# Kernel tuning notes

Measured on AMD Instinct MI355X. Metric: run time of the kernel, lower is better.

Reference implementation:

```python
import jax, jax.numpy as jnp
import numpy as np

B, T, C = 4, 2048, 1024
N_HEAD = 16
HS = C // N_HEAD  # head_size = 64


def setup_inputs() -> dict:
    key = jax.random.key(0)
    k1, k2, k3 = jax.random.split(key, 3)
    x = jax.random.normal(k1, (B, T, C), dtype=jnp.float32)
    # torch Linear(in, out, bias=False); stored here as (in, out) so y = x @ W
    W_attn = jax.random.normal(k2, (C, 3 * C), dtype=jnp.float32) * (C ** -0.5)
    W_proj = jax.random.normal(k3, (C, C), dtype=jnp.float32) * (C ** -0.5)
    return {"x": x, "W_attn": W_attn, "W_proj": W_proj}


def reference(x, W_attn, W_proj):
    Bq, Tq, Cq = x.shape
    qkv = x @ W_attn                              # (B, T, 3C)
    q, k, v = jnp.split(qkv, 3, axis=-1)          # each (B, T, C)
    # (B, T, C) -> (B, H, T, hs)
    q = q.reshape(Bq, Tq, N_HEAD, HS).transpose(0, 2, 1, 3)
    k = k.reshape(Bq, Tq, N_HEAD, HS).transpose(0, 2, 1, 3)
    v = v.reshape(Bq, Tq, N_HEAD, HS).transpose(0, 2, 1, 3)
    scale = HS ** -0.5
    att = jnp.einsum("bhqd,bhkd->bhqk", q, k) * scale  # (B, H, T, T)
    causal = jnp.tril(jnp.ones((Tq, Tq), dtype=bool))
    att = jnp.where(causal[None, None], att, jnp.finfo(att.dtype).min)
    att = jax.nn.softmax(att, axis=-1)
    y = jnp.einsum("bhqk,bhkd->bhqd", att, v)     # (B, H, T, hs)
    y = y.transpose(0, 2, 1, 3).reshape(Bq, Tq, Cq)
    return y @ W_proj                             # (B, T, C)
```

## Files before the change

kernel.cpp:

```cpp
#include <hip/hip_runtime.h>
#include <stdint.h>

typedef __bf16 bf16x8 __attribute__((ext_vector_type(8)));
typedef float f32x4 __attribute__((ext_vector_type(4)));

__device__ __forceinline__ unsigned short f2bf(float f) {
  unsigned u = __builtin_bit_cast(unsigned, f);
  u = (u + 0x7fffu + ((u >> 16) & 1u)) >> 16;
  return (unsigned short)u;
}

__device__ __forceinline__ unsigned cvt_pk_bf16(float a, float b) {
  unsigned r;
  asm("v_cvt_pk_bf16_f32 %0, %1, %2" : "=v"(r) : "v"(a), "v"(b));
  return r;
}

__device__ __forceinline__ void gload_lds16(const unsigned short* g, unsigned short* l) {
  __builtin_amdgcn_global_load_lds(
      (__attribute__((address_space(1))) unsigned int*)g,
      (__attribute__((address_space(3))) unsigned int*)l, 16, 0, 0);
}

__device__ __forceinline__ void store_val(float* p, float v) { *p = v; }
__device__ __forceinline__ void store_val(unsigned short* p, float v) { *p = f2bf(v); }

__device__ __forceinline__ void transpose_tile(const float* __restrict__ in,
                                               unsigned short* __restrict__ out,
                                               int R, int Ccols, float qscale, int qcols,
                                               int bxx, int byy,
                                               unsigned short (*t)[65]) {
  int r0 = byy * 64, c0 = bxx * 64;
  int tid = threadIdx.x;
#pragma unroll
  for (int rep = 0; rep < 16; rep++) {
    int idx = rep * 256 + tid;
    int rr = idx >> 6, cc = idx & 63;
    float v = in[(size_t)(r0 + rr) * Ccols + c0 + cc];
    if (c0 + cc < qcols) v *= qscale;
    t[rr][cc] = f2bf(v);
  }
  __syncthreads();
#pragma unroll
  for (int rep = 0; rep < 16; rep++) {
    int idx = rep * 256 + tid;
    int cc = idx >> 6, rr = idx & 63;
    out[(size_t)(c0 + cc) * R + r0 + rr] = t[rr][cc];
  }
}

__global__ __launch_bounds__(256) void prep_kernel(const float* __restrict__ x,
                                                   unsigned short* __restrict__ xb,
                                                   const float* __restrict__ Wa,
                                                   unsigned short* __restrict__ Wta,
                                                   const float* __restrict__ Wp,
                                                   unsigned short* __restrict__ Wtp,
                                                   float SC) {
  __shared__ unsigned short t[64][65];
  int bx = blockIdx.x;
  if (bx < 2048) {
    const int n = 8192 * 1024;
    const int stride = 2048 * 256 * 4;
    for (int i = (bx * 256 + threadIdx.x) * 4; i < n; i += stride) {
      float4 v = *(const float4*)(x + i);
      ushort4 o;
      o.x = f2bf(v.x); o.y = f2bf(v.y); o.z = f2bf(v.z); o.w = f2bf(v.w);
      *(ushort4*)(xb + i) = o;
    }
  } else if (bx < 2816) {
    int idx = bx - 2048;
    transpose_tile(Wa, Wta, 1024, 3072, SC, 1024, idx % 48, idx / 48, t);
  } else {
    int idx = bx - 2816;
    transpose_tile(Wp, Wtp, 1024, 1024, 1.0f, 0, idx % 16, idx / 16, t);
  }
}

template <typename OutT, bool WRITEV>
__global__ __launch_bounds__(512, 2) void gemm_bt(const unsigned short* __restrict__ A,
                                                  const unsigned short* __restrict__ Bt,
                                                  OutT* __restrict__ C, int M, int N, int K,
                                                  int mtiles, unsigned short* __restrict__ vt) {
  __shared__ unsigned short lds3[3][24576];
  const int tid = threadIdx.x;
  const int wid = tid >> 6, l = tid & 63;
  const int wm = wid >> 2, wn = wid & 3;
  const int lr = l & 15, lg = l >> 4;

  int nwg = gridDim.x;
  int q8 = nwg >> 3;
  int bid = blockIdx.x;
  int bs = (bid & 7) * q8 + (bid >> 3);
  int mt = bs % mtiles, nt = bs / mtiles;
  const int m0 = mt * 128, n0 = nt * 256;

  const int srow = tid >> 3;
  const int schunk = ((tid & 7) ^ (srow & 7)) * 8;
  const unsigned short* gA0 = A + (size_t)(m0 + srow) * K + schunk;
  const unsigned short* gB0 = Bt + (size_t)(n0 + srow) * K + schunk;
  const int wslice = wid * 512;

  int arow[4], brow[2][2], xoff[2];
#pragma unroll
  for (int m = 0; m < 4; m++) arow[m] = (wm * 64 + m * 16 + lr) * 64;
#pragma unroll
  for (int qq = 0; qq < 2; qq++)
#pragma unroll
    for (int j = 0; j < 2; j++) brow[qq][j] = 8192 + (wn * 64 + qq * 32 + j * 16 + lr) * 64;
#pragma unroll
  for (int ks = 0; ks < 2; ks++) xoff[ks] = ((ks * 4 + lg) ^ (lr & 7)) * 8;

  f32x4 acc[4][4] = {};
  const int NT = K >> 6;

  gload_lds16(gA0, &lds3[0][wslice]);
  gload_lds16(gA0 + (size_t)64 * K, &lds3[0][4096 + wslice]);
#pragma unroll
  for (int u = 0; u < 4; u++)
    gload_lds16(gB0 + (size_t)(u * 64) * K, &lds3[0][8192 + u * 4096 + wslice]);
  gload_lds16(gA0 + 64, &lds3[1][wslice]);
  gload_lds16(gA0 + (size_t)64 * K + 64, &lds3[1][4096 + wslice]);
#pragma unroll
  for (int u = 0; u < 4; u++)
    gload_lds16(gB0 + (size_t)(u * 64) * K + 64, &lds3[1][8192 + u * 4096 + wslice]);

  int cb = 0;
  for (int t = 0; t < NT; t++) {
    if (t == NT - 1) {
      asm volatile("s_waitcnt vmcnt(0)" ::: "memory");
    } else {
      asm volatile("s_waitcnt vmcnt(6)" ::: "memory");
    }
    __builtin_amdgcn_s_barrier();
    const unsigned short* bufc = lds3[cb];
    int pb = cb + 2; if (pb >= 3) pb -= 3;
    unsigned short* bufp = lds3[pb];
    const int k2 = (t + 2) * 64;
    const bool pre = (t + 2) < NT;

    if (pre) {
      gload_lds16(gA0 + k2, bufp + wslice);
      gload_lds16(gA0 + (size_t)64 * K + k2, bufp + 4096 + wslice);
      gload_lds16(gB0 + k2, bufp + 8192 + wslice);
    }
    bf16x8 af[4][2];
#pragma unroll
    for (int m = 0; m < 4; m++)
#pragma unroll
      for (int ks = 0; ks < 2; ks++)
        af[m][ks] = *(const bf16x8*)&bufc[arow[m] + xoff[ks]];
    {
      bf16x8 bq[2][2];
#pragma unroll
      for (int j = 0; j < 2; j++)
#pragma unroll
        for (int ks = 0; ks < 2; ks++)
          bq[j][ks] = *(const bf16x8*)&bufc[brow[0][j] + xoff[ks]];
      __builtin_amdgcn_s_setprio(1);
#pragma unroll
      for (int m = 0; m < 4; m++)
#pragma unroll
        for (int j = 0; j < 2; j++)
#pragma unroll
          for (int ks = 0; ks < 2; ks++)
            acc[m][j] = __builtin_amdgcn_mfma_f32_16x16x32_bf16(af[m][ks], bq[j][ks], acc[m][j], 0, 0, 0);
      __builtin_amdgcn_s_setprio(0);
    }
    if (pre) {
      gload_lds16(gB0 + (size_t)64 * K + k2, bufp + 12288 + wslice);
      gload_lds16(gB0 + (size_t)128 * K + k2, bufp + 16384 + wslice);
      gload_lds16(gB0 + (size_t)192 * K + k2, bufp + 20480 + wslice);
    }
    {
      bf16x8 bq[2][2];
#pragma unroll
      for (int j = 0; j < 2; j++)
#pragma unroll
        for (int ks = 0; ks < 2; ks++)
          bq[j][ks] = *(const bf16x8*)&bufc[brow[1][j] + xoff[ks]];
      __builtin_amdgcn_s_setprio(1);
#pragma unroll
      for (int m = 0; m < 4; m++)
#pragma unroll
        for (int j = 0; j < 2; j++)
#pragma unroll
          for (int ks = 0; ks < 2; ks++)
            acc[m][2 + j] = __builtin_amdgcn_mfma_f32_16x16x32_bf16(af[m][ks], bq[j][ks], acc[m][2 + j], 0, 0, 0);
      __builtin_amdgcn_s_setprio(0);
    }
    cb = (cb == 2) ? 0 : cb + 1;
  }

  if (WRITEV && n0 >= 2048) {
    int hh = ((n0 - 2048) >> 6) + wn;
#pragma unroll
    for (int m = 0; m < 4; m++) {
      int row = m0 + wm * 64 + m * 16 + lg * 4;
      int bb = row >> 11, tt = row & 2047;
      size_t base = (size_t)(bb * 16 + hh) * 131072 + tt;
#pragma unroll
      for (int n = 0; n < 4; n++) {
        int d = n * 16 + lr;
        ushort4 v;
        v.x = f2bf(acc[m][n][0]); v.y = f2bf(acc[m][n][1]);
        v.z = f2bf(acc[m][n][2]); v.w = f2bf(acc[m][n][3]);
        *(ushort4*)&vt[base + (size_t)d * 2048] = v;
      }
    }
  } else {
#pragma unroll
    for (int m = 0; m < 4; m++)
#pragma unroll
      for (int n = 0; n < 4; n++)
#pragma unroll
        for (int i = 0; i < 4; i++) {
          size_t row = (size_t)(m0 + wm * 64 + m * 16 + lg * 4 + i);
          size_t col = (size_t)(n0 + wn * 64 + n * 16 + lr);
          store_val(&C[row * N + col], acc[m][n][i]);
        }
  }
}

__global__ __launch_bounds__(256, 3) void attn_kernel(const unsigned short* __restrict__ qkv,
                                                      const unsigned short* __restrict__ vt,
                                                      unsigned short* __restrict__ y) {
  __shared__ unsigned short k_lds[2][64 * 64];
  __shared__ unsigned short v_lds[2][64 * 64];
  __shared__ unsigned short p_lds[8][16 * 64];
  int tid = threadIdx.x;
  int w = tid >> 6, l = tid & 63;
  int lr = l & 15, lg = l >> 4;
  int g4 = lg * 4;
  int lband = l & 48;
  int bh = blockIdx.x;
  int b = bh >> 4, h = bh & 15;
  int qgrp = 15 - blockIdx.y;
  int q0 = qgrp * 128 + w * 32;

  char* plo = (char*)p_lds[w * 2];
  char* phi = (char*)p_lds[w * 2 + 1];

  int srow = tid >> 3;
  int schunk = (tid & 7) ^ (srow & 7);
  const unsigned short* gK0 = qkv + (size_t)(b * 2048 + srow) * 3072 + 1024 + h * 64 + schunk * 8;
  const unsigned short* gK1 = gK0 + (size_t)32 * 3072;
  const unsigned short* gV0 = vt + (size_t)bh * 131072 + (size_t)srow * 2048 + schunk * 8;
  const unsigned short* gV1 = gV0 + (size_t)32 * 2048;
  int ldsbase0 = w * 512;
  int ldsbase1 = 2048 + w * 512;

  const unsigned short* qp = qkv + (size_t)(b * 2048 + q0 + lr) * 3072 + h * 64 + lg * 8;
  bf16x8 aQ0lo = *(const bf16x8*)qp;
  bf16x8 aQ1lo = *(const bf16x8*)(qp + 32);
  bf16x8 aQ0hi = *(const bf16x8*)(qp + 16 * 3072);
  bf16x8 aQ1hi = *(const bf16x8*)(qp + 16 * 3072 + 32);

  f32x4 Olo[4] = {}, Ohi[4] = {};
  float sumlo = 0.f, sumhi = 0.f;

  int rx = lr & 7;
  int kc0 = (lg ^ rx) * 8;
  int kc1 = ((4 + lg) ^ rx) * 8;

  int nbmax = ((qgrp * 128 + 96) >> 6) + 1;
  int kend = q0 + 31;
  int kdiag = q0 >> 6;

  gload_lds16(gK0, &k_lds[0][ldsbase0]);
  gload_lds16(gK1, &k_lds[0][ldsbase1]);
  gload_lds16(gV0, &v_lds[0][ldsbase0]);
  gload_lds16(gV1, &v_lds[0][ldsbase1]);
  __syncthreads();

  int cur = 0;
  for (int kb = 0; kb < nbmax; kb++) {
    int kbase = kb * 64;
    if (kb + 1 < nbmax) {
      size_t koff = (size_t)(kbase + 64) * 3072;
      size_t voff = (size_t)(kbase + 64);
      int nxt = cur ^ 1;
      gload_lds16(gK0 + koff, &k_lds[nxt][ldsbase0]);
      gload_lds16(gK1 + koff, &k_lds[nxt][ldsbase1]);
      gload_lds16(gV0 + voff, &v_lds[nxt][ldsbase0]);
      gload_lds16(gV1 + voff, &v_lds[nxt][ldsbase1]);
    }
    if (kbase <= kend) {
      const unsigned short* kl = k_lds[cur];
      const unsigned short* vl = v_lds[cur];
      f32x4 svlo[4], svhi[4];
      __builtin_amdgcn_s_setprio(1);
#pragma unroll
      for (int n = 0; n < 4; n++) {
        bf16x8 kf0 = *(const bf16x8*)&kl[(n * 16 + lr) * 64 + kc0];
        bf16x8 kf1 = *(const bf16x8*)&kl[(n * 16 + lr) * 64 + kc1];
        f32x4 z = {};
        z = __builtin_amdgcn_mfma_f32_16x16x32_bf16(kf0, aQ0lo, z, 0, 0, 0);
        z = __builtin_amdgcn_mfma_f32_16x16x32_bf16(kf1, aQ1lo, z, 0, 0, 0);
        svlo[n] = z;
        f32x4 z2 = {};
        z2 = __builtin_amdgcn_mfma_f32_16x16x32_bf16(kf0, aQ0hi, z2, 0, 0, 0);
        z2 = __builtin_amdgcn_mfma_f32_16x16x32_bf16(kf1, aQ1hi, z2, 0, 0, 0);
        svhi[n] = z2;
      }
      __builtin_amdgcn_s_setprio(0);
      if (kb == kdiag) {
#pragma unroll
        for (int n = 0; n < 4; n++)
#pragma unroll
          for (int i = 0; i < 4; i++) {
            int kk = kbase + n * 16 + g4 + i;
            if (kk > q0 + lr) svlo[n][i] = -1.0e38f;
            if (kk > q0 + 16 + lr) svhi[n][i] = -1.0e38f;
          }
      }
      float pslo = 0.f, pshi = 0.f;
      unsigned pk0lo[4], pk1lo[4], pk0hi[4], pk1hi[4];
#pragma unroll
      for (int n = 0; n < 4; n++) {
        float a0 = __builtin_amdgcn_exp2f(svlo[n][0]);
        float a1 = __builtin_amdgcn_exp2f(svlo[n][1]);
        float a2 = __builtin_amdgcn_exp2f(svlo[n][2]);
        float a3 = __builtin_amdgcn_exp2f(svlo[n][3]);
        pslo += (a0 + a1) + (a2 + a3);
        pk0lo[n] = cvt_pk_bf16(a0, a1);
        pk1lo[n] = cvt_pk_bf16(a2, a3);
        float c0 = __builtin_amdgcn_exp2f(svhi[n][0]);
        float c1 = __builtin_amdgcn_exp2f(svhi[n][1]);
        float c2 = __builtin_amdgcn_exp2f(svhi[n][2]);
        float c3 = __builtin_amdgcn_exp2f(svhi[n][3]);
        pshi += (c0 + c1) + (c2 + c3);
        pk0hi[n] = cvt_pk_bf16(c0, c1);
        pk1hi[n] = cvt_pk_bf16(c2, c3);
      }
      pslo += __shfl_xor(pslo, 16);
      pslo += __shfl_xor(pslo, 32);
      pshi += __shfl_xor(pshi, 16);
      pshi += __shfl_xor(pshi, 32);
      sumlo += pslo;
      sumhi += pshi;
#pragma unroll
      for (int n = 0; n < 4; n++) {
        int chunk = (2 * n + (lg >> 1)) ^ rx;
        int off = lr * 128 + chunk * 16 + (lg & 1) * 8;
        *(uint2*)(plo + off) = make_uint2(pk0lo[n], pk1lo[n]);
        *(uint2*)(phi + off) = make_uint2(pk0hi[n], pk1hi[n]);
      }
      bf16x8 aPlo0 = *(const bf16x8*)(plo + lr * 128 + (lg ^ rx) * 16);
      bf16x8 aPlo1 = *(const bf16x8*)(plo + lr * 128 + ((4 + lg) ^ rx) * 16);
      bf16x8 aPhi0 = *(const bf16x8*)(phi + lr * 128 + (lg ^ rx) * 16);
      bf16x8 aPhi1 = *(const bf16x8*)(phi + lr * 128 + ((4 + lg) ^ rx) * 16);
      __builtin_amdgcn_s_setprio(1);
#pragma unroll
      for (int n2 = 0; n2 < 4; n2++) {
        bf16x8 v0 = *(const bf16x8*)&vl[(n2 * 16 + lr) * 64 + kc0];
        bf16x8 v1 = *(const bf16x8*)&vl[(n2 * 16 + lr) * 64 + kc1];
        Olo[n2] = __builtin_amdgcn_mfma_f32_16x16x32_bf16(aPlo0, v0, Olo[n2], 0, 0, 0);
        Olo[n2] = __builtin_amdgcn_mfma_f32_16x16x32_bf16(aPlo1, v1, Olo[n2], 0, 0, 0);
        Ohi[n2] = __builtin_amdgcn_mfma_f32_16x16x32_bf16(aPhi0, v0, Ohi[n2], 0, 0, 0);
        Ohi[n2] = __builtin_amdgcn_mfma_f32_16x16x32_bf16(aPhi1, v1, Ohi[n2], 0, 0, 0);
      }
      __builtin_amdgcn_s_setprio(0);
    }
    __syncthreads();
    cur ^= 1;
  }
  float s0 = __shfl(sumlo, lband | g4);
  float s1 = __shfl(sumlo, lband | (g4 + 1));
  float s2 = __shfl(sumlo, lband | (g4 + 2));
  float s3 = __shfl(sumlo, lband | (g4 + 3));
  float t0 = __shfl(sumhi, lband | g4);
  float t1 = __shfl(sumhi, lband | (g4 + 1));
  float t2 = __shfl(sumhi, lband | (g4 + 2));
  float t3 = __shfl(sumhi, lband | (g4 + 3));
  float rl0 = 1.f / s0, rl1 = 1.f / s1, rl2 = 1.f / s2, rl3 = 1.f / s3;
  float rh0 = 1.f / t0, rh1 = 1.f / t1, rh2 = 1.f / t2, rh3 = 1.f / t3;
#pragma unroll
  for (int n2 = 0; n2 < 4; n2++) {
    size_t base = (size_t)(b * 2048 + q0 + g4) * 1024 + h * 64 + n2 * 16 + lr;
    y[base] = f2bf(Olo[n2][0] * rl0);
    y[base + 1024] = f2bf(Olo[n2][1] * rl1);
    y[base + 2048] = f2bf(Olo[n2][2] * rl2);
    y[base + 3072] = f2bf(Olo[n2][3] * rl3);
    size_t bhh = base + (size_t)16 * 1024;
    y[bhh] = f2bf(Ohi[n2][0] * rh0);
    y[bhh + 1024] = f2bf(Ohi[n2][1] * rh1);
    y[bhh + 2048] = f2bf(Ohi[n2][2] * rh2);
    y[bhh + 3072] = f2bf(Ohi[n2][3] * rh3);
  }
}

extern "C" void kernel_launch(void* const* d_in, const int* in_sizes, int n_in,
                              void* d_out, int out_size, void* d_ws, size_t ws_size,
                              hipStream_t stream) {
  const float* x = (const float*)d_in[0];
  const float* Wa = (const float*)d_in[1];
  const float* Wp = (const float*)d_in[2];
  float* out = (float*)d_out;

  char* ws = (char*)d_ws;
  size_t off = 0;
  unsigned short* xb = (unsigned short*)(ws + off);   off += (size_t)8192 * 1024 * 2;
  unsigned short* Wta = (unsigned short*)(ws + off);  off += (size_t)3072 * 1024 * 2;
  unsigned short* Wtp = (unsigned short*)(ws + off);  off += (size_t)1024 * 1024 * 2;
  unsigned short* qkvb = (unsigned short*)(ws + off); off += (size_t)8192 * 3072 * 2;
  unsigned short* vtb = (unsigned short*)(ws + off);  off += (size_t)64 * 64 * 2048 * 2;
  unsigned short* yb = (unsigned short*)(ws + off);   off += (size_t)8192 * 1024 * 2;

  const float SC = 0.125f * 1.44269504f;
  prep_kernel<<<3072, 256, 0, stream>>>(x, xb, Wa, Wta, Wp, Wtp, SC);
  gemm_bt<unsigned short, true><<<768, 512, 0, stream>>>(xb, Wta, qkvb, 8192, 3072, 1024, 64, vtb);
  attn_kernel<<<dim3(64, 16), 256, 0, stream>>>(qkvb, vtb, yb);
  gemm_bt<float, false><<<256, 512, 0, stream>>>(yb, Wtp, out, 8192, 1024, 1024, 64, nullptr);
}
```

Before: 159.5 us.

## Add dedicated 256x256-tile QKV GEMM with double-buffered LDS

Adds a specialized QKV projection kernel that uses 256x256 output tiles (8x4 MFMA accumulators per wave) in place of 128x256, with a two-stage LDS double buffer in place of the three-stage ring. It also hardcodes K/N and the tile swizzle. The larger tile raises arithmetic intensity and halves the number of workgroups (384 instead of 768), cutting redundant global loads of A and B. In exchange it uses more registers and 128KB of LDS per block, which may limit occupancy. Fewer workgroups also means only 384 blocks spread across the CUs. The output projection GEMM is simplified to a float-only variant.

```diff
diff --git a/kernel.cpp b/kernel.cpp
--- a/kernel.cpp
+++ b/kernel.cpp
@@ -76,11 +76,140 @@
   }
 }
 
-template <typename OutT, bool WRITEV>
+__global__ __launch_bounds__(512, 2) void gemm_qkv(const unsigned short* __restrict__ A,
+                                                   const unsigned short* __restrict__ Bt,
+                                                   unsigned short* __restrict__ C,
+                                                   unsigned short* __restrict__ vt) {
+  const int K = 1024, N = 3072, NT = 16;
+  __shared__ unsigned short lds[2][32768];
+  const int tid = threadIdx.x;
+  const int wid = tid >> 6, l = tid & 63;
+  const int wm = wid >> 2, wn = wid & 3;
+  const int lr = l & 15, lg = l >> 4;
+
+  int bid = blockIdx.x;
+  int bs = (bid & 7) * 48 + (bid >> 3);
+  int mt = bs & 31, nt = bs >> 5;
+  const int m0 = mt * 256, n0 = nt * 256;
+
+  const int srow = tid >> 3;
+  const int schunk = ((tid & 7) ^ (srow & 7)) * 8;
+  const unsigned short* gA0 = A + (size_t)(m0 + srow) * K + schunk;
+  const unsigned short* gB0 = Bt + (size_t)(n0 + srow) * K + schunk;
+  const int dst = tid * 8;
+
+  int arow[8], brow[4], xoff[2];
+#pragma unroll
+  for (int m = 0; m < 8; m++) arow[m] = (wm * 128 + m * 16 + lr) * 64;
+#pragma unroll
+  for (int n = 0; n < 4; n++) brow[n] = 16384 + (wn * 64 + n * 16 + lr) * 64;
+#pragma unroll
+  for (int ks = 0; ks < 2; ks++) xoff[ks] = ((ks * 4 + lg) ^ (lr & 7)) * 8;
+
+  f32x4 acc[8][4] = {};
+
+#pragma unroll
+  for (int u = 0; u < 4; u++)
+    gload_lds16(gA0 + (size_t)(u * 64) * K, &lds[0][u * 4096 + dst]);
+#pragma unroll
+  for (int u = 0; u < 4; u++)
+    gload_lds16(gB0 + (size_t)(u * 64) * K, &lds[0][16384 + u * 4096 + dst]);
+
+  int cur = 0;
+  for (int t = 0; t < NT; t++) {
+    if (t + 1 < NT) {
+      int k1 = (t + 1) * 64;
+      unsigned short* bp = lds[cur ^ 1];
+#pragma unroll
+      for (int u = 0; u < 4; u++)
+        gload_lds16(gA0 + (size_t)(u * 64) * K + k1, bp + u * 4096 + dst);
+#pragma unroll
+      for (int u = 0; u < 4; u++)
+        gload_lds16(gB0 + (size_t)(u * 64) * K + k1, bp + 16384 + u * 4096 + dst);
+      asm volatile("s_waitcnt vmcnt(8)" ::: "memory");
+    } else {
+      asm volatile("s_waitcnt vmcnt(0)" ::: "memory");
+    }
+    __builtin_amdgcn_s_barrier();
+    const unsigned short* bufc = lds[cur];
+    bf16x8 bq[4][2];
+#pragma unroll
+    for (int n = 0; n < 4; n++)
+#pragma unroll
+      for (int ks = 0; ks < 2; ks++)
+        bq[n][ks] = *(const bf16x8*)&bufc[brow[n] + xoff[ks]];
+    {
+      bf16x8 af[4][2];
+#pragma unroll
+      for (int m = 0; m < 4; m++)
+#pragma unroll
+        for (int ks = 0; ks < 2; ks++)
+          af[m][ks] = *(const bf16x8*)&bufc[arow[m] + xoff[ks]];
+      __builtin_amdgcn_s_setprio(1);
+#pragma unroll
+      for (int m = 0; m < 4; m++)
+#pragma unroll
+        for (int n = 0; n < 4; n++)
+#pragma unroll
+          for (int ks = 0; ks < 2; ks++)
+            acc[m][n] = __builtin_amdgcn_mfma_f32_16x16x32_bf16(af[m][ks], bq[n][ks], acc[m][n], 0, 0, 0);
+      __builtin_amdgcn_s_setprio(0);
+    }
+    {
+      bf16x8 af[4][2];
+#pragma unroll
+      for (int m = 0; m < 4; m++)
+#pragma unroll
+        for (int ks = 0; ks < 2; ks++)
+          af[m][ks] = *(const bf16x8*)&bufc[arow[4 + m] + xoff[ks]];
+      __builtin_amdgcn_s_setprio(1);
+#pragma unroll
+      for (int m = 0; m < 4; m++)
+#pragma unroll
+        for (int n = 0; n < 4; n++)
+#pragma unroll
+          for (int ks = 0; ks < 2; ks++)
+            acc[4 + m][n] = __builtin_amdgcn_mfma_f32_16x16x32_bf16(af[m][ks], bq[n][ks], acc[4 + m][n], 0, 0, 0);
+      __builtin_amdgcn_s_setprio(0);
+    }
+    __builtin_amdgcn_s_barrier();
+    cur ^= 1;
+  }
+
+  if (n0 >= 2048) {
+    int hh = ((n0 - 2048) >> 6) + wn;
+#pragma unroll
+    for (int m = 0; m < 8; m++) {
+      int row = m0 + wm * 128 + m * 16 + lg * 4;
+      int bb = row >> 11, tt = row & 2047;
+      size_t base = (size_t)(bb * 16 + hh) * 131072 + tt;
+#pragma unroll
+      for (int n = 0; n < 4; n++) {
+        int d = n * 16 + lr;
+        ushort4 v;
+        v.x = f2bf(acc[m][n][0]); v.y = f2bf(acc[m][n][1]);
+        v.z = f2bf(acc[m][n][2]); v.w = f2bf(acc[m][n][3]);
+        *(ushort4*)&vt[base + (size_t)d * 2048] = v;
+      }
+    }
+  } else {
+#pragma unroll
+    for (int m = 0; m < 8; m++)
+#pragma unroll
+      for (int n = 0; n < 4; n++)
+#pragma unroll
+        for (int i = 0; i < 4; i++) {
+          size_t row = (size_t)(m0 + wm * 128 + m * 16 + lg * 4 + i);
+          size_t col = (size_t)(n0 + wn * 64 + n * 16 + lr);
+          C[row * N + col] = f2bf(acc[m][n][i]);
+        }
+  }
+}
+
 __global__ __launch_bounds__(512, 2) void gemm_bt(const unsigned short* __restrict__ A,
                                                   const unsigned short* __restrict__ Bt,
-                                                  OutT* __restrict__ C, int M, int N, int K,
-                                                  int mtiles, unsigned short* __restrict__ vt) {
+                                                  float* __restrict__ C, int M, int N, int K,
+                                                  int mtiles) {
   __shared__ unsigned short lds3[3][24576];
   const int tid = threadIdx.x;
   const int wid = tid >> 6, l = tid & 63;
@@ -191,34 +320,16 @@
     cb = (cb == 2) ? 0 : cb + 1;
   }
 
-  if (WRITEV && n0 >= 2048) {
-    int hh = ((n0 - 2048) >> 6) + wn;
-#pragma unroll
-    for (int m = 0; m < 4; m++) {
-      int row = m0 + wm * 64 + m * 16 + lg * 4;
-      int bb = row >> 11, tt = row & 2047;
-      size_t base = (size_t)(bb * 16 + hh) * 131072 + tt;
-#pragma unroll
-      for (int n = 0; n < 4; n++) {
-        int d = n * 16 + lr;
-        ushort4 v;
-        v.x = f2bf(acc[m][n][0]); v.y = f2bf(acc[m][n][1]);
-        v.z = f2bf(acc[m][n][2]); v.w = f2bf(acc[m][n][3]);
-        *(ushort4*)&vt[base + (size_t)d * 2048] = v;
-      }
-    }
-  } else {
-#pragma unroll
-    for (int m = 0; m < 4; m++)
-#pragma unroll
-      for (int n = 0; n < 4; n++)
-#pragma unroll
-        for (int i = 0; i < 4; i++) {
-          size_t row = (size_t)(m0 + wm * 64 + m * 16 + lg * 4 + i);
-          size_t col = (size_t)(n0 + wn * 64 + n * 16 + lr);
-          store_val(&C[row * N + col], acc[m][n][i]);
-        }
-  }
+#pragma unroll
+  for (int m = 0; m < 4; m++)
+#pragma unroll
+    for (int n = 0; n < 4; n++)
+#pragma unroll
+      for (int i = 0; i < 4; i++) {
+        size_t row = (size_t)(m0 + wm * 64 + m * 16 + lg * 4 + i);
+        size_t col = (size_t)(n0 + wn * 64 + n * 16 + lr);
+        C[row * N + col] = acc[m][n][i];
+      }
 }
 
 __global__ __launch_bounds__(256, 3) void attn_kernel(const unsigned short* __restrict__ qkv,
@@ -408,7 +519,7 @@
 
   const float SC = 0.125f * 1.44269504f;
   prep_kernel<<<3072, 256, 0, stream>>>(x, xb, Wa, Wta, Wp, Wtp, SC);
-  gemm_bt<unsigned short, true><<<768, 512, 0, stream>>>(xb, Wta, qkvb, 8192, 3072, 1024, 64, vtb);
+  gemm_qkv<<<384, 512, 0, stream>>>(xb, Wta, qkvb, vtb);
   attn_kernel<<<dim3(64, 16), 256, 0, stream>>>(qkvb, vtb, yb);
-  gemm_bt<float, false><<<256, 512, 0, stream>>>(yb, Wtp, out, 8192, 1024, 1024, 64, nullptr);
-}
+  gemm_bt<<<256, 512, 0, stream>>>(yb, Wtp, out, 8192, 1024, 1024, 64);
+}
```

Result: slower. 171.1 us (+7.2%).
